# Optimization experiments

Measured on AMD Instinct MI355X. Metric: run time of the kernel, lower is better.

Reference implementation:

```python
import jax, jax.numpy as jnp
import numpy as np

B, C, H, W = 8, 256, 128, 128
SH, SW = 8, 8            # stoken_size
HH, WW = H // SH, W // SW
NH = 8                   # num_heads
HD = C // NH             # head_dim = 32
KD = HD                  # key_dim (attn_ratio=1)
ATTN_SCALE = KD ** (-0.5)
AFF_SCALE = C ** (-0.5)


def unfold9(x):
    """x: (B,C,hh,ww) -> (B, hh*ww, C, 9); matches Unfold(3) + transpose/reshape."""
    b, c, hh, ww = x.shape
    xp = jnp.pad(x, ((0, 0), (0, 0), (1, 1), (1, 1)))
    p = jnp.stack([xp[:, :, dy:dy + hh, dx:dx + ww]
                   for dy in range(3) for dx in range(3)], axis=2)  # (B,C,9,hh,ww)
    return p.transpose(0, 3, 4, 1, 2).reshape(b, hh * ww, c, 9)


def fold9(y):
    """y: (B,C,9,hh,ww) -> (B,C,hh,ww); matches Fold(3) (conv_transpose with identity kernels)."""
    hh, ww = y.shape[-2:]
    yp = jnp.pad(y, ((0, 0), (0, 0), (0, 0), (1, 1), (1, 1)))
    out = 0.
    for dy in range(3):
        for dx in range(3):
            out = out + yp[:, :, dy * 3 + dx, 2 - dy:2 - dy + hh, 2 - dx:2 - dx + ww]
    return out


def attention(sf, w_qkv, w_pe, w_proj):
    """Attention module with attn_ratio=1 (Conv layers have act=False, BN identity)."""
    b, c, hh, ww = sf.shape
    n = hh * ww
    qkv = jnp.einsum('oc,bchw->bohw', w_qkv, sf).reshape(b, NH, 2 * KD + HD, n)
    q, k, v = jnp.split(qkv, [KD, 2 * KD], axis=2)
    attn = jax.nn.softmax(jnp.einsum('bhkn,bhkm->bhnm', q, k) * ATTN_SCALE, axis=-1)
    o = jnp.einsum('bhdm,bhnm->bhdn', v, attn).reshape(b, c, hh, ww)
    pe = jax.lax.conv_general_dilated(
        v.reshape(b, c, hh, ww), w_pe, (1, 1), ((1, 1), (1, 1)),
        dimension_numbers=('NCHW', 'OIHW', 'NCHW'), feature_group_count=c)
    return jnp.einsum('oc,bchw->bohw', w_proj, o + pe)


def setup_inputs() -> dict:
    key = jax.random.key(0)
    k0, k1, k2, k3 = jax.random.split(key, 4)
    x = jax.random.normal(k0, (B, C, H, W), dtype=jnp.float32)
    w_qkv = jax.random.normal(k1, (3 * C, C), dtype=jnp.float32) * 0.05
    w_pe = jax.random.normal(k2, (C, 1, 3, 3), dtype=jnp.float32) * 0.05
    w_proj = jax.random.normal(k3, (C, C), dtype=jnp.float32) * 0.05
    return {'x': x, 'w_qkv': w_qkv, 'w_pe': w_pe, 'w_proj': w_proj}


def reference(x, w_qkv, w_pe, w_proj):
    # H,W divisible by stoken_size -> no padding branch
    xb = x.reshape(B, C, HH, SH, WW, SW)
    stoken = xb.mean(axis=(3, 5))                                   # (B,C,hh,ww) adaptive_avg_pool2d
    pix = xb.transpose(0, 2, 4, 3, 5, 1).reshape(B, HH * WW, SH * SW, C)
    # --- single no-grad iteration (n_iter=1) ---
    sf9 = unfold9(stoken)                                            # (B,n,C,9)
    aff = jax.nn.softmax(jnp.einsum('bnpc,bnck->bnpk', pix, sf9) * AFF_SCALE, axis=-1)
    aff = jax.lax.stop_gradient(aff)                                 # torch.no_grad
    asum = aff.sum(axis=2).transpose(0, 2, 1).reshape(B, 1, 9, HH, WW)
    asum = jax.lax.stop_gradient(fold9(asum))                        # (B,1,hh,ww)
    # --- super-token aggregation ---
    sf = jnp.einsum('bnpc,bnpk->bnck', pix, aff)                     # (B,n,C,9)
    sf = fold9(sf.transpose(0, 2, 3, 1).reshape(B, C, 9, HH, WW))    # (B,C,hh,ww)
    sf = sf / (asum + 1e-12)
    # --- refine with attention ---
    sf = attention(sf, w_qkv, w_pe, w_proj)
    # --- scatter back to pixels ---
    sf9b = unfold9(sf)                                               # (B,n,C,9)
    pix_out = jnp.einsum('bnck,bnpk->bnpc', sf9b, aff)               # (B,n,h*w,C)
    return pix_out.reshape(B, HH, WW, C, SH, SW).transpose(0, 3, 1, 4, 2, 5).reshape(B, C, H, W)
```

## Files before the change

### kernel.cpp

```cpp
#include <hip/hip_runtime.h>
#include <cstdint>
#include <cstddef>


#define AFF_SCALE 0.0625f
#define ATTN_SCALE 0.17677669529663687f

__device__ __forceinline__ float dpp_add_xor1(float v) {
    int p = __builtin_amdgcn_update_dpp(0, __float_as_int(v), 0xB1, 0xF, 0xF, true);
    return v + __int_as_float(p);
}
__device__ __forceinline__ float dpp_add_xor2(float v) {
    int p = __builtin_amdgcn_update_dpp(0, __float_as_int(v), 0x4E, 0xF, 0xF, true);
    return v + __int_as_float(p);
}

__global__ __launch_bounds__(128) void stoken_kernel(
    const float* __restrict__ x, float* __restrict__ stok_pad)
{
    int blk = blockIdx.x;
    int i  = blk & 15;
    int bc = blk >> 4;
    int t  = threadIdx.x;
    const float* xr = x + ((size_t)bc * 128 + i * 8) * 128 + t;
    float s = 0.f;
#pragma unroll
    for (int r = 0; r < 8; ++r) s += xr[r * 128];
    s += __shfl_down(s, 4, 64);
    s += __shfl_down(s, 2, 64);
    s += __shfl_down(s, 1, 64);
    if ((t & 7) == 0) {
        int j = t >> 3;
        int b = bc >> 8, c = bc & 255;
        stok_pad[(((size_t)b * 18 + (i + 1)) * 18 + (j + 1)) * 256 + c] =
            s * (1.f / 64.f);
    }
}

__global__ __launch_bounds__(256, 4) void aff_agg_kernel(
    const float* __restrict__ x, const float* __restrict__ stok_pad,
    float* __restrict__ aff_g, float* __restrict__ asum_g,
    float* __restrict__ agg)
{
    __shared__ __align__(16) float sfs[9 * 260];
    __shared__ __align__(16) float part[576];
    __shared__ __align__(16) float affs[576];

    int bid  = blockIdx.x;
    int xcd  = bid & 7, slot_ = bid >> 3;
    int pair = xcd * 128 + (slot_ >> 1);
    int m = pair & 7, i = (pair >> 3) & 15, b = pair >> 7;
    int j = m * 2 + (slot_ & 1);
    int bn = b * 256 + i * 16 + j;
    int t = threadIdx.x;

    {
        const float* spT = stok_pad + (size_t)b * 324 * 256;
#pragma unroll
        for (int dy = 0; dy < 3; ++dy)
#pragma unroll
            for (int dx = 0; dx < 3; ++dx) {
                int r = i + dy, cn = j + dx;
                float v = 0.f;
                if ((unsigned)(r - 1) < 16u && (unsigned)(cn - 1) < 16u)
                    v = spT[((size_t)r * 18 + cn) * 256 + t];
                sfs[(dy * 3 + dx) * 260 + t] = v;
            }
    }
    part[t] = 0.f;
    part[t + 256] = 0.f;
    if (t < 64) part[t + 512] = 0.f;
    __syncthreads();

    int w = t >> 6, l = t & 63;

    {
        int pq = l >> 2, cgl = l & 3;
        int cbase = w * 64 + cgl * 16;
        int pi = pq >> 1, pj4 = (pq & 1) * 4;
        const float* xb = x + (size_t)(b * 256) * 16384
                            + (size_t)(i * 8 + pi) * 128 + j * 8 + pj4;
        float acc[4][9];
#pragma unroll
        for (int ii = 0; ii < 4; ++ii)
#pragma unroll
            for (int k = 0; k < 9; ++k) acc[ii][k] = 0.f;

#pragma unroll
        for (int c4i = 0; c4i < 4; ++c4i) {
            int c = cbase + c4i * 4;
            const float4 p0 = *(const float4*)&xb[(size_t)(c + 0) * 16384];
            const float4 p1 = *(const float4*)&xb[(size_t)(c + 1) * 16384];
            const float4 p2 = *(const float4*)&xb[(size_t)(c + 2) * 16384];
            const float4 p3 = *(const float4*)&xb[(size_t)(c + 3) * 16384];
#pragma unroll
            for (int k = 0; k < 9; ++k) {
                const float4 sv = *(const float4*)&sfs[k * 260 + c];
                acc[0][k] += p0.x * sv.x + p1.x * sv.y + p2.x * sv.z + p3.x * sv.w;
                acc[1][k] += p0.y * sv.x + p1.y * sv.y + p2.y * sv.z + p3.y * sv.w;
                acc[2][k] += p0.z * sv.x + p1.z * sv.y + p2.z * sv.z + p3.z * sv.w;
                acc[3][k] += p0.w * sv.x + p1.w * sv.y + p2.w * sv.z + p3.w * sv.w;
            }
        }
#pragma unroll
        for (int ii = 0; ii < 4; ++ii)
#pragma unroll
            for (int k = 0; k < 9; ++k) {
                acc[ii][k] = dpp_add_xor1(acc[ii][k]);
                acc[ii][k] = dpp_add_xor2(acc[ii][k]);
            }
#pragma unroll
        for (int k = 0; k < 9; ++k) {
            float v01 = (cgl & 1) ? acc[1][k] : acc[0][k];
            float v23 = (cgl & 1) ? acc[3][k] : acc[2][k];
            float vk  = (cgl & 2) ? v23 : v01;
            atomicAdd(&part[l * 9 + k], vk);
        }
    }
    __syncthreads();

    if (t < 64) {
        float a[9];
        float mx = -1e30f;
#pragma unroll
        for (int k = 0; k < 9; ++k) {
            float v = part[t * 9 + k] * AFF_SCALE;
            a[k] = v;
            mx = fmaxf(mx, v);
        }
        float ssum = 0.f;
#pragma unroll
        for (int k = 0; k < 9; ++k) { a[k] = __expf(a[k] - mx); ssum += a[k]; }
        float inv = 1.f / ssum;
#pragma unroll
        for (int k = 0; k < 9; ++k) {
            a[k] *= inv;
            affs[k * 64 + t] = a[k];
            aff_g[(size_t)bn * 576 + k * 64 + t] = a[k];
        }
#pragma unroll
        for (int k = 0; k < 9; ++k) {
            float r = a[k];
            r += __shfl_down(r, 32, 64); r += __shfl_down(r, 16, 64);
            r += __shfl_down(r, 8, 64);  r += __shfl_down(r, 4, 64);
            r += __shfl_down(r, 2, 64);  r += __shfl_down(r, 1, 64);
            if (t == 0) asum_g[(size_t)bn * 9 + k] = r;
        }
    }
    __syncthreads();

    {
        int cql = l >> 2, pq2 = l & 3;
        int cb2 = w * 64 + cql * 4;
        const float* xb = x + (size_t)(b * 256) * 16384 + (size_t)(i * 8) * 128 + j * 8;
        float acc2[4][9];
#pragma unroll
        for (int ii = 0; ii < 4; ++ii)
#pragma unroll
            for (int k = 0; k < 9; ++k) acc2[ii][k] = 0.f;

#pragma unroll
        for (int pp = 0; pp < 4; ++pp) {
            int p4 = pq2 * 4 + pp;
            int pi = p4 >> 1, pj4 = (p4 & 1) * 4;
            const float* xr = xb + (size_t)pi * 128 + pj4;
            const float4 q0 = *(const float4*)&xr[(size_t)(cb2 + 0) * 16384];
            const float4 q1 = *(const float4*)&xr[(size_t)(cb2 + 1) * 16384];
            const float4 q2 = *(const float4*)&xr[(size_t)(cb2 + 2) * 16384];
            const float4 q3 = *(const float4*)&xr[(size_t)(cb2 + 3) * 16384];
#pragma unroll
            for (int k = 0; k < 9; ++k) {
                const float4 av = *(const float4*)&affs[k * 64 + p4 * 4];
                acc2[0][k] += q0.x * av.x + q0.y * av.y + q0.z * av.z + q0.w * av.w;
                acc2[1][k] += q1.x * av.x + q1.y * av.y + q1.z * av.z + q1.w * av.w;
                acc2[2][k] += q2.x * av.x + q2.y * av.y + q2.z * av.z + q2.w * av.w;
                acc2[3][k] += q3.x * av.x + q3.y * av.y + q3.z * av.z + q3.w * av.w;
            }
        }
#pragma unroll
        for (int ii = 0; ii < 4; ++ii)
#pragma unroll
            for (int k = 0; k < 9; ++k) {
                acc2[ii][k] = dpp_add_xor1(acc2[ii][k]);
                acc2[ii][k] = dpp_add_xor2(acc2[ii][k]);
            }
        int cout = w * 64 + l;
#pragma unroll
        for (int k = 0; k < 9; ++k) {
            float v01 = (pq2 & 1) ? acc2[1][k] : acc2[0][k];
            float v23 = (pq2 & 1) ? acc2[3][k] : acc2[2][k];
            float vk  = (pq2 & 2) ? v23 : v01;
            agg[((size_t)bn * 9 + k) * 256 + cout] = vk;
        }
    }
}

__global__ __launch_bounds__(256) void fold_div_kernel(
    const float* __restrict__ agg, const float* __restrict__ asum_g,
    float* __restrict__ sf)
{
    __shared__ float v[256 * 17];
    int b = blockIdx.x >> 4, y = blockIdx.x & 15;
    int t = threadIdx.x;
    for (int x = 0; x < 16; ++x) {
        float af = 0.f, val = 0.f;
#pragma unroll
        for (int dy = 0; dy < 3; ++dy)
#pragma unroll
            for (int dx = 0; dx < 3; ++dx) {
                int ii = y + 1 - dy, jj = x + 1 - dx;
                if ((unsigned)ii < 16u && (unsigned)jj < 16u) {
                    int idx = (b * 256 + ii * 16 + jj) * 9 + dy * 3 + dx;
                    af  += asum_g[idx];
                    val += agg[(size_t)idx * 256 + t];
                }
            }
        v[t * 17 + x] = val / (af + 1e-12f);
    }
    __syncthreads();
    int xw = t & 15, cw0 = t >> 4;
#pragma unroll
    for (int it = 0; it < 16; ++it) {
        int c = cw0 + it * 16;
        sf[((size_t)b * 256 + c) * 256 + y * 16 + xw] = v[c * 17 + xw];
    }
}

__global__ __launch_bounds__(256) void gemm_w(
    const float* __restrict__ A, const float* __restrict__ Bm,
    float* __restrict__ Cout, int M)
{
    __shared__ float As[32 * 68];
    __shared__ float Bs[32 * 64];
    int b = blockIdx.x, o0 = blockIdx.y * 64, n0 = blockIdx.z * 64;
    int t = threadIdx.x;
    int tr = t >> 4, tc = t & 15;
    const float* Bb = Bm + (size_t)b * 256 * 256;
    float acc[4][4];
#pragma unroll
    for (int ii = 0; ii < 4; ++ii)
#pragma unroll
        for (int jj = 0; jj < 4; ++jj) acc[ii][jj] = 0.f;

    for (int k0 = 0; k0 < 256; k0 += 32) {
        {
            int ol = t >> 2, kq = (t & 3) * 8;
            const float* Ap = A + (size_t)(o0 + ol) * 256 + k0 + kq;
            const float4 f0 = *(const float4*)&Ap[0];
            const float4 f1 = *(const float4*)&Ap[4];
            As[(kq + 0) * 68 + ol] = f0.x; As[(kq + 1) * 68 + ol] = f0.y;
            As[(kq + 2) * 68 + ol] = f0.z; As[(kq + 3) * 68 + ol] = f0.w;
            As[(kq + 4) * 68 + ol] = f1.x; As[(kq + 5) * 68 + ol] = f1.y;
            As[(kq + 6) * 68 + ol] = f1.z; As[(kq + 7) * 68 + ol] = f1.w;
        }
#pragma unroll
        for (int i2 = 0; i2 < 8; ++i2) {
            int e = t + i2 * 256;
            int kl = e >> 6, nl = e & 63;
            Bs[kl * 64 + nl] = Bb[(size_t)(k0 + kl) * 256 + n0 + nl];
        }
        __syncthreads();
#pragma unroll
        for (int kk = 0; kk < 32; ++kk) {
            const float4 av = *(const float4*)&As[kk * 68 + tr * 4];
            const float4 bv = *(const float4*)&Bs[kk * 64 + tc * 4];
            acc[0][0] += av.x * bv.x; acc[0][1] += av.x * bv.y; acc[0][2] += av.x * bv.z; acc[0][3] += av.x * bv.w;
            acc[1][0] += av.y * bv.x; acc[1][1] += av.y * bv.y; acc[1][2] += av.y * bv.z; acc[1][3] += av.y * bv.w;
            acc[2][0] += av.z * bv.x; acc[2][1] += av.z * bv.y; acc[2][2] += av.z * bv.z; acc[2][3] += av.z * bv.w;
            acc[3][0] += av.w * bv.x; acc[3][1] += av.w * bv.y; acc[3][2] += av.w * bv.z; acc[3][3] += av.w * bv.w;
        }
        __syncthreads();
    }

#pragma unroll
    for (int ii = 0; ii < 4; ++ii) {
        int o = o0 + tr * 4 + ii;
        float4 st = make_float4(acc[ii][0], acc[ii][1], acc[ii][2], acc[ii][3]);
        *(float4*)&Cout[((size_t)b * M + o) * 256 + n0 + tc * 4] = st;
    }
}

__global__ __launch_bounds__(256) void gemm_proj32(
    const float* __restrict__ A, const float* __restrict__ Bm,
    float* __restrict__ Cout)
{
    __shared__ float As[32 * 36];
    __shared__ float Bs[32 * 64];
    int b = blockIdx.x, o0 = blockIdx.y * 32, n0 = blockIdx.z * 64;
    int t = threadIdx.x;
    int tr = t >> 4, tc = t & 15;
    const float* Bb = Bm + (size_t)b * 256 * 256;
    float acc[2][4];
#pragma unroll
    for (int ii = 0; ii < 2; ++ii)
#pragma unroll
        for (int jj = 0; jj < 4; ++jj) acc[ii][jj] = 0.f;

    for (int k0 = 0; k0 < 256; k0 += 32) {
        {
            int ol = t & 31, kq = (t >> 5) * 4;
            const float* Ap = A + (size_t)(o0 + ol) * 256 + k0 + kq;
            const float4 f = *(const float4*)&Ap[0];
            As[(kq + 0) * 36 + ol] = f.x; As[(kq + 1) * 36 + ol] = f.y;
            As[(kq + 2) * 36 + ol] = f.z; As[(kq + 3) * 36 + ol] = f.w;
        }
#pragma unroll
        for (int i2 = 0; i2 < 8; ++i2) {
            int e = t + i2 * 256;
            int kl = e >> 6, nl = e & 63;
            Bs[kl * 64 + nl] = Bb[(size_t)(k0 + kl) * 256 + n0 + nl];
        }
        __syncthreads();
#pragma unroll
        for (int kk = 0; kk < 32; ++kk) {
            const float2 av = *(const float2*)&As[kk * 36 + tr * 2];
            const float4 bv = *(const float4*)&Bs[kk * 64 + tc * 4];
            acc[0][0] += av.x * bv.x; acc[0][1] += av.x * bv.y;
            acc[0][2] += av.x * bv.z; acc[0][3] += av.x * bv.w;
            acc[1][0] += av.y * bv.x; acc[1][1] += av.y * bv.y;
            acc[1][2] += av.y * bv.z; acc[1][3] += av.y * bv.w;
        }
        __syncthreads();
    }

#pragma unroll
    for (int jj = 0; jj < 4; ++jj) {
        int n = n0 + tc * 4 + jj;
        int y = n >> 4, x = n & 15;
        float2 st = make_float2(acc[0][jj], acc[1][jj]);
        *(float2*)&Cout[(((size_t)b * 18 + 1 + y) * 18 + 1 + x) * 256 + o0 + tr * 2] = st;
    }
}

__global__ __launch_bounds__(256) void attn_kernel(
    const float* __restrict__ qkv, float* __restrict__ o_attn)
{
    __shared__ float smem[9216];
    int b = blockIdx.x, h = blockIdx.y, nt = blockIdx.z;
    int t = threadIdx.x, nl = t & 31, mq = t >> 5;
    int n = nt * 32 + nl;

    {
        int dd = t >> 3, mb = (t & 7) * 32;
        const float* krow = qkv + ((size_t)b * 768 + h * 96 + 32 + dd) * 256;
#pragma unroll
        for (int e4 = 0; e4 < 8; ++e4) {
            int m = mb + e4 * 4;
            const float4 kw = *(const float4*)&krow[m];
            smem[(m + 0) * 32 + dd] = kw.x; smem[(m + 1) * 32 + dd] = kw.y;
            smem[(m + 2) * 32 + dd] = kw.z; smem[(m + 3) * 32 + dd] = kw.w;
        }
    }
    float q[32];
    {
        const float* qbase = qkv + ((size_t)b * 768 + h * 96) * 256 + n;
#pragma unroll
        for (int d = 0; d < 32; ++d) q[d] = qbase[(size_t)d * 256];
    }
    __syncthreads();

    float l[32];
#pragma unroll
    for (int e = 0; e < 32; ++e) {
        const float* kp = &smem[(mq * 32 + e) * 32];
        float s = 0.f;
#pragma unroll
        for (int d4 = 0; d4 < 8; ++d4) {
            const float4 kv4 = *(const float4*)&kp[d4 * 4];
            s += q[d4 * 4 + 0] * kv4.x + q[d4 * 4 + 1] * kv4.y +
                 q[d4 * 4 + 2] * kv4.z + q[d4 * 4 + 3] * kv4.w;
        }
        l[e] = s * ATTN_SCALE;
    }
    float mx = -1e30f;
#pragma unroll
    for (int e = 0; e < 32; ++e) mx = fmaxf(mx, l[e]);
    float sm = 0.f;
#pragma unroll
    for (int e = 0; e < 32; ++e) { l[e] = __expf(l[e] - mx); sm += l[e]; }
    __syncthreads();

    {
        int dd = t >> 3, mb = (t & 7) * 32;
        const float* vrow = qkv + ((size_t)b * 768 + h * 96 + 64 + dd) * 256;
#pragma unroll
        for (int e4 = 0; e4 < 8; ++e4) {
            int m = mb + e4 * 4;
            const float4 vw = *(const float4*)&vrow[m];
            smem[(m + 0) * 32 + dd] = vw.x; smem[(m + 1) * 32 + dd] = vw.y;
            smem[(m + 2) * 32 + dd] = vw.z; smem[(m + 3) * 32 + dd] = vw.w;
        }
    }
    __syncthreads();

    float oa[32];
#pragma unroll
    for (int d = 0; d < 32; ++d) oa[d] = 0.f;
#pragma unroll
    for (int e = 0; e < 32; ++e) {
        float pm = l[e];
        const float* vp = &smem[(mq * 32 + e) * 32];
#pragma unroll
        for (int d4 = 0; d4 < 8; ++d4) {
            const float4 vv = *(const float4*)&vp[d4 * 4];
            oa[d4 * 4 + 0] += pm * vv.x; oa[d4 * 4 + 1] += pm * vv.y;
            oa[d4 * 4 + 2] += pm * vv.z; oa[d4 * 4 + 3] += pm * vv.w;
        }
    }
    __syncthreads();

    float* op   = smem;
    float* mxsm = smem + 8448;
    {
        int idx = mq * 32 + nl;
#pragma unroll
        for (int d = 0; d < 32; ++d) op[idx * 33 + d] = oa[d];
        mxsm[idx * 2 + 0] = mx;
        mxsm[idx * 2 + 1] = sm;
    }
    __syncthreads();

    if (t < 32) {
        float M2 = -1e30f;
#pragma unroll
        for (int q8 = 0; q8 < 8; ++q8) M2 = fmaxf(M2, mxsm[(q8 * 32 + t) * 2]);
        float w[8], S = 0.f;
#pragma unroll
        for (int q8 = 0; q8 < 8; ++q8) {
            w[q8] = __expf(mxsm[(q8 * 32 + t) * 2] - M2);
            S += mxsm[(q8 * 32 + t) * 2 + 1] * w[q8];
        }
        float inv = 1.f / S;
#pragma unroll
        for (int d = 0; d < 32; ++d) {
            float o = 0.f;
#pragma unroll
            for (int q8 = 0; q8 < 8; ++q8) o += op[(q8 * 32 + t) * 33 + d] * w[q8];
            o_attn[((size_t)b * 256 + h * 32 + d) * 256 + nt * 32 + t] = o * inv;
        }
    }
}

__global__ __launch_bounds__(256) void peadd_kernel(
    const float* __restrict__ qkv, const float* __restrict__ w_pe,
    float* __restrict__ o_attn)
{
    int bc = blockIdx.x;
    int b = bc >> 8, c = bc & 255;
    int t = threadIdx.x;
    int y = t >> 4, x = t & 15;
    int h = c >> 5, d = c & 31;
    const float* v = qkv + ((size_t)b * 768 + h * 96 + 64 + d) * 256;
    float acc = o_attn[(size_t)bc * 256 + t];
#pragma unroll
    for (int ky = 0; ky < 3; ++ky)
#pragma unroll
        for (int kx = 0; kx < 3; ++kx) {
            int yy = y + ky - 1, xx = x + kx - 1;
            if ((unsigned)yy < 16u && (unsigned)xx < 16u)
                acc += w_pe[c * 9 + ky * 3 + kx] * v[yy * 16 + xx];
        }
    o_attn[(size_t)bc * 256 + t] = acc;
}

__global__ __launch_bounds__(256) void scatter_kernel(
    const float* __restrict__ sfa_pad, const float* __restrict__ aff_g,
    float* __restrict__ out)
{
    __shared__ float ss[3 * 18 * 40];
    __shared__ float aff_s[16 * 577];

    int blk = blockIdx.x;
    int pi = blk & 7, i = (blk >> 3) & 15, b = blk >> 7;
    int t = threadIdx.x;

    for (int e = t; e < 1728; e += 256) {
        int dy = e / 576, rem = e % 576;
        int col = rem >> 5, idx = rem & 31;
        int q = idx >> 3, d = idx & 7;
        int row = i + dy;
        float v = 0.f;
        if ((unsigned)(row - 1) < 16u && (unsigned)(col - 1) < 16u)
            v = sfa_pad[(((size_t)b * 18 + row) * 18 + col) * 256 + q * 64 + pi * 8 + d];
        ss[(dy * 18 + col) * 40 + idx] = v;
    }
    {
        const float* ag = aff_g + ((size_t)b * 256 + i * 16) * 576;
        for (int e = t; e < 9216; e += 256) {
            int j = e / 576, rem = e % 576;
            int k = rem >> 6, p = rem & 63;
            aff_s[j * 577 + p * 9 + k] = ag[j * 576 + rem];
        }
    }
    __syncthreads();

    int lane = t & 63, w = t >> 6;
    int j0 = lane >> 3, pj = lane & 7;
    int j1 = j0 + 8;

    float S0[4][9], S1[4][9];
#pragma unroll
    for (int q = 0; q < 4; ++q)
#pragma unroll
        for (int k = 0; k < 9; ++k) {
            int dy = k / 3, dx = k % 3;
            S0[q][k] = ss[(dy * 18 + j0 + dx) * 40 + q * 8 + pj];
            S1[q][k] = ss[(dy * 18 + j1 + dx) * 40 + q * 8 + pj];
        }

    int y = i * 8 + pi;
    size_t ob = (size_t)b * 256 * 16384 + (size_t)y * 128;
    const float* A0 = &aff_s[j0 * 577];
    const float* A1 = &aff_s[j1 * 577];
    for (int p = w * 16; p < w * 16 + 16; ++p) {
        float a0[9], a1[9];
#pragma unroll
        for (int k = 0; k < 9; ++k) { a0[k] = A0[p * 9 + k]; a1[k] = A1[p * 9 + k]; }
#pragma unroll
        for (int q = 0; q < 4; ++q) {
            int c2 = p * 4 + q;
            float v0 = 0.f, v1 = 0.f;
#pragma unroll
            for (int k = 0; k < 9; ++k) {
                v0 += S0[q][k] * a0[k];
                v1 += S1[q][k] * a1[k];
            }
            out[ob + (size_t)c2 * 16384 + lane] = v0;
            out[ob + (size_t)c2 * 16384 + 64 + lane] = v1;
        }
    }
}

extern "C" void kernel_launch(void* const* d_in, const int* in_sizes, int n_in,
                              void* d_out, int out_size, void* d_ws, size_t ws_size,
                              hipStream_t stream) {
    const float* x      = (const float*)d_in[0];
    const float* w_qkv  = (const float*)d_in[1];
    const float* w_pe   = (const float*)d_in[2];
    const float* w_proj = (const float*)d_in[3];
    float* out = (float*)d_out;
    float* agg = (float*)d_out;

    float* ws = (float*)d_ws;
    const size_t o_aff  = 0;
    const size_t o_asum = 1179648;
    const size_t o_pad  = 1198080;
    const size_t o_sf   = 1861632;
    const size_t o_qkv  = 2385920;

    stoken_kernel<<<8 * 256 * 16, 128, 0, stream>>>(x, ws + o_pad);
    aff_agg_kernel<<<8 * 256, 256, 0, stream>>>(x, ws + o_pad, ws + o_aff,
                                                ws + o_asum, agg);
    fold_div_kernel<<<8 * 16, 256, 0, stream>>>(agg, ws + o_asum, ws + o_sf);
    gemm_w<<<dim3(8, 12, 4), 256, 0, stream>>>(w_qkv, ws + o_sf, ws + o_qkv, 768);
    attn_kernel<<<dim3(8, 8, 8), 256, 0, stream>>>(ws + o_qkv, ws + o_sf);
    peadd_kernel<<<8 * 256, 256, 0, stream>>>(ws + o_qkv, w_pe, ws + o_sf);
    gemm_proj32<<<dim3(8, 8, 4), 256, 0, stream>>>(w_proj, ws + o_sf, ws + o_pad);
    scatter_kernel<<<8 * 16 * 8, 256, 0, stream>>>(ws + o_pad, ws + o_aff, out);
}
```

Before: 434.6 us.

## Fuse positional-encoding conv into attention, split fold grid, unify GEMMs with 32-row tiles

The depthwise 3x3 positional-encoding conv is folded into the attention kernel's epilogue, which reuses the V tile already held in shared memory, so the separate peadd kernel and its read-modify-write of o_attn go away. fold_div now splits channels across twice as many blocks to raise parallelism. The QKV GEMM switches to the 32-row tile kernel, giving more blocks, and one mode flag selects its output layout. The attention kernel uses more shared memory because its buffers are no longer aliased, which may reduce occupancy.

```diff
diff --git a/kernel.cpp b/kernel.cpp
--- a/kernel.cpp
+++ b/kernel.cpp
@@ -199,10 +199,13 @@
     const float* __restrict__ agg, const float* __restrict__ asum_g,
     float* __restrict__ sf)
 {
-    __shared__ float v[256 * 17];
-    int b = blockIdx.x >> 4, y = blockIdx.x & 15;
+    __shared__ float v[128 * 17];
+    int bid = blockIdx.x;
+    int b = bid >> 5, y = (bid >> 1) & 15, ch = bid & 1;
     int t = threadIdx.x;
-    for (int x = 0; x < 16; ++x) {
+    int cl = t & 127, xp = t >> 7;
+    for (int it = 0; it < 8; ++it) {
+        int x = it * 2 + xp;
         float af = 0.f, val = 0.f;
 #pragma unroll
         for (int dy = 0; dy < 3; ++dy)
@@ -212,77 +215,24 @@
                 if ((unsigned)ii < 16u && (unsigned)jj < 16u) {
                     int idx = (b * 256 + ii * 16 + jj) * 9 + dy * 3 + dx;
                     af  += asum_g[idx];
-                    val += agg[(size_t)idx * 256 + t];
+                    val += agg[(size_t)idx * 256 + ch * 128 + cl];
                 }
             }
-        v[t * 17 + x] = val / (af + 1e-12f);
-    }
-    __syncthreads();
-    int xw = t & 15, cw0 = t >> 4;
-#pragma unroll
-    for (int it = 0; it < 16; ++it) {
-        int c = cw0 + it * 16;
-        sf[((size_t)b * 256 + c) * 256 + y * 16 + xw] = v[c * 17 + xw];
-    }
-}
-
-__global__ __launch_bounds__(256) void gemm_w(
+        v[cl * 17 + x] = val / (af + 1e-12f);
+    }
+    __syncthreads();
+    int xw = t & 15, cw = t >> 4;
+#pragma unroll
+    for (int itc = 0; itc < 8; ++itc) {
+        int c_local = cw + itc * 16;
+        sf[((size_t)b * 256 + ch * 128 + c_local) * 256 + y * 16 + xw] =
+            v[c_local * 17 + xw];
+    }
+}
+
+__global__ __launch_bounds__(256) void gemm32(
     const float* __restrict__ A, const float* __restrict__ Bm,
-    float* __restrict__ Cout, int M)
-{
-    __shared__ float As[32 * 68];
-    __shared__ float Bs[32 * 64];
-    int b = blockIdx.x, o0 = blockIdx.y * 64, n0 = blockIdx.z * 64;
-    int t = threadIdx.x;
-    int tr = t >> 4, tc = t & 15;
-    const float* Bb = Bm + (size_t)b * 256 * 256;
-    float acc[4][4];
-#pragma unroll
-    for (int ii = 0; ii < 4; ++ii)
-#pragma unroll
-        for (int jj = 0; jj < 4; ++jj) acc[ii][jj] = 0.f;
-
-    for (int k0 = 0; k0 < 256; k0 += 32) {
-        {
-            int ol = t >> 2, kq = (t & 3) * 8;
-            const float* Ap = A + (size_t)(o0 + ol) * 256 + k0 + kq;
-            const float4 f0 = *(const float4*)&Ap[0];
-            const float4 f1 = *(const float4*)&Ap[4];
-            As[(kq + 0) * 68 + ol] = f0.x; As[(kq + 1) * 68 + ol] = f0.y;
-            As[(kq + 2) * 68 + ol] = f0.z; As[(kq + 3) * 68 + ol] = f0.w;
-            As[(kq + 4) * 68 + ol] = f1.x; As[(kq + 5) * 68 + ol] = f1.y;
-            As[(kq + 6) * 68 + ol] = f1.z; As[(kq + 7) * 68 + ol] = f1.w;
-        }
-#pragma unroll
-        for (int i2 = 0; i2 < 8; ++i2) {
-            int e = t + i2 * 256;
-            int kl = e >> 6, nl = e & 63;
-            Bs[kl * 64 + nl] = Bb[(size_t)(k0 + kl) * 256 + n0 + nl];
-        }
-        __syncthreads();
-#pragma unroll
-        for (int kk = 0; kk < 32; ++kk) {
-            const float4 av = *(const float4*)&As[kk * 68 + tr * 4];
-            const float4 bv = *(const float4*)&Bs[kk * 64 + tc * 4];
-            acc[0][0] += av.x * bv.x; acc[0][1] += av.x * bv.y; acc[0][2] += av.x * bv.z; acc[0][3] += av.x * bv.w;
-            acc[1][0] += av.y * bv.x; acc[1][1] += av.y * bv.y; acc[1][2] += av.y * bv.z; acc[1][3] += av.y * bv.w;
-            acc[2][0] += av.z * bv.x; acc[2][1] += av.z * bv.y; acc[2][2] += av.z * bv.z; acc[2][3] += av.z * bv.w;
-            acc[3][0] += av.w * bv.x; acc[3][1] += av.w * bv.y; acc[3][2] += av.w * bv.z; acc[3][3] += av.w * bv.w;
-        }
-        __syncthreads();
-    }
-
-#pragma unroll
-    for (int ii = 0; ii < 4; ++ii) {
-        int o = o0 + tr * 4 + ii;
-        float4 st = make_float4(acc[ii][0], acc[ii][1], acc[ii][2], acc[ii][3]);
-        *(float4*)&Cout[((size_t)b * M + o) * 256 + n0 + tc * 4] = st;
-    }
-}
-
-__global__ __launch_bounds__(256) void gemm_proj32(
-    const float* __restrict__ A, const float* __restrict__ Bm,
-    float* __restrict__ Cout)
+    float* __restrict__ Cout, int M, int mode)
 {
     __shared__ float As[32 * 36];
     __shared__ float Bs[32 * 64];
@@ -323,19 +273,32 @@
         __syncthreads();
     }
 
-#pragma unroll
-    for (int jj = 0; jj < 4; ++jj) {
-        int n = n0 + tc * 4 + jj;
-        int y = n >> 4, x = n & 15;
-        float2 st = make_float2(acc[0][jj], acc[1][jj]);
-        *(float2*)&Cout[(((size_t)b * 18 + 1 + y) * 18 + 1 + x) * 256 + o0 + tr * 2] = st;
+    if (mode == 0) {
+#pragma unroll
+        for (int ii = 0; ii < 2; ++ii) {
+            int o = o0 + tr * 2 + ii;
+            float4 st = make_float4(acc[ii][0], acc[ii][1], acc[ii][2], acc[ii][3]);
+            *(float4*)&Cout[((size_t)b * M + o) * 256 + n0 + tc * 4] = st;
+        }
+    } else {
+#pragma unroll
+        for (int jj = 0; jj < 4; ++jj) {
+            int n = n0 + tc * 4 + jj;
+            int y = n >> 4, x = n & 15;
+            float2 st = make_float2(acc[0][jj], acc[1][jj]);
+            *(float2*)&Cout[(((size_t)b * 18 + 1 + y) * 18 + 1 + x) * 256 + o0 + tr * 2] = st;
+        }
     }
 }
 
 __global__ __launch_bounds__(256) void attn_kernel(
-    const float* __restrict__ qkv, float* __restrict__ o_attn)
+    const float* __restrict__ qkv, const float* __restrict__ w_pe,
+    float* __restrict__ o_attn)
 {
-    __shared__ float smem[9216];
+    __shared__ float kv[8192];
+    __shared__ float op[256 * 33];
+    __shared__ float mxsm[512];
+    __shared__ float wpe_s[288];
     int b = blockIdx.x, h = blockIdx.y, nt = blockIdx.z;
     int t = threadIdx.x, nl = t & 31, mq = t >> 5;
     int n = nt * 32 + nl;
@@ -347,10 +310,12 @@
         for (int e4 = 0; e4 < 8; ++e4) {
             int m = mb + e4 * 4;
             const float4 kw = *(const float4*)&krow[m];
-            smem[(m + 0) * 32 + dd] = kw.x; smem[(m + 1) * 32 + dd] = kw.y;
-            smem[(m + 2) * 32 + dd] = kw.z; smem[(m + 3) * 32 + dd] = kw.w;
-        }
-    }
+            kv[(m + 0) * 32 + dd] = kw.x; kv[(m + 1) * 32 + dd] = kw.y;
+            kv[(m + 2) * 32 + dd] = kw.z; kv[(m + 3) * 32 + dd] = kw.w;
+        }
+    }
+    for (int e = t; e < 288; e += 256) wpe_s[e] = w_pe[h * 288 + e];
+
     float q[32];
     {
         const float* qbase = qkv + ((size_t)b * 768 + h * 96) * 256 + n;
@@ -362,7 +327,7 @@
     float l[32];
 #pragma unroll
     for (int e = 0; e < 32; ++e) {
-        const float* kp = &smem[(mq * 32 + e) * 32];
+        const float* kp = &kv[(mq * 32 + e) * 32];
         float s = 0.f;
 #pragma unroll
         for (int d4 = 0; d4 < 8; ++d4) {
@@ -387,8 +352,8 @@
         for (int e4 = 0; e4 < 8; ++e4) {
             int m = mb + e4 * 4;
             const float4 vw = *(const float4*)&vrow[m];
-            smem[(m + 0) * 32 + dd] = vw.x; smem[(m + 1) * 32 + dd] = vw.y;
-            smem[(m + 2) * 32 + dd] = vw.z; smem[(m + 3) * 32 + dd] = vw.w;
+            kv[(m + 0) * 32 + dd] = vw.x; kv[(m + 1) * 32 + dd] = vw.y;
+            kv[(m + 2) * 32 + dd] = vw.z; kv[(m + 3) * 32 + dd] = vw.w;
         }
     }
     __syncthreads();
@@ -399,7 +364,7 @@
 #pragma unroll
     for (int e = 0; e < 32; ++e) {
         float pm = l[e];
-        const float* vp = &smem[(mq * 32 + e) * 32];
+        const float* vp = &kv[(mq * 32 + e) * 32];
 #pragma unroll
         for (int d4 = 0; d4 < 8; ++d4) {
             const float4 vv = *(const float4*)&vp[d4 * 4];
@@ -407,10 +372,7 @@
             oa[d4 * 4 + 2] += pm * vv.z; oa[d4 * 4 + 3] += pm * vv.w;
         }
     }
-    __syncthreads();
-
-    float* op   = smem;
-    float* mxsm = smem + 8448;
+
     {
         int idx = mq * 32 + nl;
 #pragma unroll
@@ -431,36 +393,25 @@
             S += mxsm[(q8 * 32 + t) * 2 + 1] * w[q8];
         }
         float inv = 1.f / S;
+        int n2 = nt * 32 + t;
+        int y0 = n2 >> 4, x0 = n2 & 15;
 #pragma unroll
         for (int d = 0; d < 32; ++d) {
             float o = 0.f;
 #pragma unroll
             for (int q8 = 0; q8 < 8; ++q8) o += op[(q8 * 32 + t) * 33 + d] * w[q8];
-            o_attn[((size_t)b * 256 + h * 32 + d) * 256 + nt * 32 + t] = o * inv;
-        }
-    }
-}
-
-__global__ __launch_bounds__(256) void peadd_kernel(
-    const float* __restrict__ qkv, const float* __restrict__ w_pe,
-    float* __restrict__ o_attn)
-{
-    int bc = blockIdx.x;
-    int b = bc >> 8, c = bc & 255;
-    int t = threadIdx.x;
-    int y = t >> 4, x = t & 15;
-    int h = c >> 5, d = c & 31;
-    const float* v = qkv + ((size_t)b * 768 + h * 96 + 64 + d) * 256;
-    float acc = o_attn[(size_t)bc * 256 + t];
-#pragma unroll
-    for (int ky = 0; ky < 3; ++ky)
-#pragma unroll
-        for (int kx = 0; kx < 3; ++kx) {
-            int yy = y + ky - 1, xx = x + kx - 1;
-            if ((unsigned)yy < 16u && (unsigned)xx < 16u)
-                acc += w_pe[c * 9 + ky * 3 + kx] * v[yy * 16 + xx];
-        }
-    o_attn[(size_t)bc * 256 + t] = acc;
+            float pe = 0.f;
+#pragma unroll
+            for (int ky = 0; ky < 3; ++ky)
+#pragma unroll
+                for (int kx = 0; kx < 3; ++kx) {
+                    int yv = y0 + ky - 1, xv = x0 + kx - 1;
+                    if ((unsigned)yv < 16u && (unsigned)xv < 16u)
+                        pe += wpe_s[d * 9 + ky * 3 + kx] * kv[(yv * 16 + xv) * 32 + d];
+                }
+            o_attn[((size_t)b * 256 + h * 32 + d) * 256 + n2] = o * inv + pe;
+        }
+    }
 }
 
 __global__ __launch_bounds__(256) void scatter_kernel(
@@ -551,10 +502,9 @@
     stoken_kernel<<<8 * 256 * 16, 128, 0, stream>>>(x, ws + o_pad);
     aff_agg_kernel<<<8 * 256, 256, 0, stream>>>(x, ws + o_pad, ws + o_aff,
                                                 ws + o_asum, agg);
-    fold_div_kernel<<<8 * 16, 256, 0, stream>>>(agg, ws + o_asum, ws + o_sf);
-    gemm_w<<<dim3(8, 12, 4), 256, 0, stream>>>(w_qkv, ws + o_sf, ws + o_qkv, 768);
-    attn_kernel<<<dim3(8, 8, 8), 256, 0, stream>>>(ws + o_qkv, ws + o_sf);
-    peadd_kernel<<<8 * 256, 256, 0, stream>>>(ws + o_qkv, w_pe, ws + o_sf);
-    gemm_proj32<<<dim3(8, 8, 4), 256, 0, stream>>>(w_proj, ws + o_sf, ws + o_pad);
+    fold_div_kernel<<<8 * 32, 256, 0, stream>>>(agg, ws + o_asum, ws + o_sf);
+    gemm32<<<dim3(8, 24, 4), 256, 0, stream>>>(w_qkv, ws + o_sf, ws + o_qkv, 768, 0);
+    attn_kernel<<<dim3(8, 8, 8), 256, 0, stream>>>(ws + o_qkv, w_pe, ws + o_sf);
+    gemm32<<<dim3(8, 8, 4), 256, 0, stream>>>(w_proj, ws + o_sf, ws + o_pad, 256, 1);
     scatter_kernel<<<8 * 16 * 8, 256, 0, stream>>>(ws + o_pad, ws + o_aff, out);
 }
```

Result: faster. 422.8 us (-2.7%).
